# Kernel optimization log

Hardware: AMD Instinct MI355X
Metric: run time of the kernel (lower is better)

Reference implementation:

```python
import jax, jax.numpy as jnp
import numpy as np

B, L, H, NH = 2, 256, 512, 8
DH = H // NH
MAXLEN = 256           # module's max_seq_len; pe index offset
PE_ROWS = 2 * MAXLEN + 1


def _lin(x, W, b):
    # torch nn.Linear convention: y = x @ W.T + b
    return x @ W.T + b


def setup_inputs() -> dict:
    rng = jax.random.key(0)
    ks = jax.random.split(rng, 24)
    s = 0.02
    inp = {
        "key": jax.random.normal(ks[0], (B, L, H), jnp.float32),
        "query": jax.random.normal(ks[1], (B, L, H), jnp.float32),
        "value": jax.random.normal(ks[2], (B, L, H), jnp.float32),
        # learned params
        "pe": jax.random.normal(ks[3], (PE_ROWS, H), jnp.float32) * s,
        "Wf": jax.random.normal(ks[4], (H, 4 * H), jnp.float32) * s,
        "bf": jnp.zeros((H,), jnp.float32),
        "Wk": jax.random.normal(ks[5], (H, H), jnp.float32) * s,
        "bk": jnp.zeros((H,), jnp.float32),
        "Wq": jax.random.normal(ks[6], (H, H), jnp.float32) * s,
        "bq": jnp.zeros((H,), jnp.float32),
        "Wv": jax.random.normal(ks[7], (H, H), jnp.float32) * s,
        "bv": jnp.zeros((H,), jnp.float32),
        "Wr": jax.random.normal(ks[8], (H, H), jnp.float32) * s,
        "br": jnp.zeros((H,), jnp.float32),
        "Wo": jax.random.normal(ks[9], (H, H), jnp.float32) * s,  # ff_final
        "bo": jnp.zeros((H,), jnp.float32),
        "u": jax.random.normal(ks[10], (NH, DH), jnp.float32) * s,
        "v": jax.random.normal(ks[11], (NH, DH), jnp.float32) * s,
        # int inputs
        "seq_len": jax.random.randint(ks[12], (B,), 100, 200).astype(jnp.int64),
        "lex_num": jax.random.randint(ks[13], (B,), 0, 50).astype(jnp.int64),
    }
    pos_s = jax.random.randint(ks[14], (B, L), 0, 250)
    pos_e = pos_s + jax.random.randint(ks[15], (B, L), 0, 5)
    inp["pos_s"] = pos_s.astype(jnp.int64)
    inp["pos_e"] = pos_e.astype(jnp.int64)
    return inp


def reference(key, query, value, pe, Wf, bf, Wk, bk, Wq, bq, Wv, bv, Wr, br,
              Wo, bo, u, v, seq_len, lex_num, pos_s, pos_e):
    b, l, _ = key.shape
    # four relative position matrices [B, L, L]
    pos_ss = pos_s[:, :, None] - pos_s[:, None, :]
    pos_se = pos_s[:, :, None] - pos_e[:, None, :]
    pos_es = pos_e[:, :, None] - pos_s[:, None, :]
    pos_ee = pos_e[:, :, None] - pos_e[:, None, :]
    # gather pe embeddings, each [B, L, L, H]
    pe_ss = pe[pos_ss + MAXLEN]
    pe_se = pe[pos_se + MAXLEN]
    pe_es = pe[pos_es + MAXLEN]
    pe_ee = pe[pos_ee + MAXLEN]
    pe_4 = jnp.concatenate([pe_ss, pe_se, pe_es, pe_ee], axis=-1)  # [B,L,L,4H]
    rel = jax.nn.relu(_lin(pe_4, Wf, bf))                          # 'ff' fusion -> [B,L,L,H]

    q = _lin(query, Wq, bq).reshape(b, l, NH, DH).transpose(0, 2, 1, 3)  # [B,nh,L,dh]
    k = _lin(key, Wk, bk).reshape(b, l, NH, DH).transpose(0, 2, 1, 3)
    val = _lin(value, Wv, bv).reshape(b, l, NH, DH).transpose(0, 2, 1, 3)
    rel = _lin(rel, Wr, br).reshape(b, l, l, NH, DH)               # [B,L,L,nh,dh]

    A = jnp.einsum('bhid,bhjd->bhij', q, k)
    B_ = jnp.einsum('bhid,bijhd->bhij', q, rel)
    C = jnp.einsum('hd,bhjd->bhj', u, k)[:, :, None, :]
    D = jnp.einsum('hd,bijhd->bhij', v, rel)

    score = (A + B_ + C + D) / np.float32(np.sqrt(DH))
    total_len = seq_len + lex_num                                   # [B]
    mask = (jnp.arange(l)[None, :] < total_len[:, None])[:, None, None, :]
    score = jnp.where(mask, score, jnp.float32(-1e15))
    attn = jax.nn.softmax(score, axis=-1)
    out = jnp.einsum('bhij,bhjd->bhid', attn, val)                  # [B,nh,L,dh]
    out = out.transpose(0, 2, 1, 3).reshape(b, l, H)
    return _lin(out, Wo, bo)
```

## Files before the change

kernel.cpp:

```cpp
#include <hip/hip_runtime.h>
#include <hip/hip_bf16.h>

typedef unsigned short USHORT;
typedef long long LL;
typedef short s8v __attribute__((ext_vector_type(8)));
typedef float f32x4 __attribute__((ext_vector_type(4)));


__device__ __forceinline__ float bf2f(USHORT u) {
  union { unsigned int i; float f; } v; v.i = ((unsigned int)u) << 16; return v.f;
}
__device__ __forceinline__ USHORT f2bf(float f) {
  unsigned int x = __float_as_uint(f);
  return (USHORT)((x + 0x7fffu + ((x >> 16) & 1u)) >> 16);
}

struct PrepArgs {
  const void* fsrc[18]; USHORT* fdst[18]; int fn[18];
  const void* wr_src; USHORT* wrT;
  const void* isrc[4]; int* idst[4];
};

__global__ __launch_bounds__(256) void prep_k(PrepArgs a, const void* qraw, int* flags) {
  __shared__ int s_w;
  const int t = threadIdx.x;
  if (t == 0) s_w = 0;
  __syncthreads();
  const USHORT* qb = (const USHORT*)qraw;
  int wild = 0;
  for (int c = t; c < 512; c += 256) {
    float x = bf2f(qb[c]);
    if (!(fabsf(x) <= 1024.0f)) wild = 1;
  }
  if (wild) atomicAdd(&s_w, 1);
  __syncthreads();
  const int f = (s_w == 0) ? 1 : 0;

  const int y = blockIdx.y;
  if (y < 18) {
    const int n = a.fn[y];
    const USHORT* sb = (const USHORT*)a.fsrc[y];
    const float* sf = (const float*)a.fsrc[y];
    USHORT* d = a.fdst[y];
    for (int idx = blockIdx.x * 256 + t; idx < n; idx += gridDim.x * 256)
      d[idx] = f ? sb[idx] : f2bf(sf[idx]);
  } else if (y == 18) {
    const USHORT* sb = (const USHORT*)a.wr_src;
    const float* sf = (const float*)a.wr_src;
    for (int idx = blockIdx.x * 256 + t; idx < 262144; idx += gridDim.x * 256) {
      const int e = idx >> 9, dd = idx & 511;
      const int s = dd * 512 + e;
      a.wrT[idx] = f ? sb[s] : f2bf(sf[s]);
    }
  } else if (blockIdx.x == 0) {
    if (t == 0) flags[0] = f;
    const int fi = (((const int*)a.isrc[0])[1] == 0) ? 1 : 0;
    if (t < 2) {
      a.idst[0][t] = fi ? (int)((const LL*)a.isrc[0])[t] : ((const int*)a.isrc[0])[t];
      a.idst[1][t] = fi ? (int)((const LL*)a.isrc[1])[t] : ((const int*)a.isrc[1])[t];
    }
    for (int c = t; c < 512; c += 256) {
      a.idst[2][c] = fi ? (int)((const LL*)a.isrc[2])[c] : ((const int*)a.isrc[2])[c];
      a.idst[3][c] = fi ? (int)((const LL*)a.isrc[3])[c] : ((const int*)a.isrc[3])[c];
    }
  }
}

struct GDesc {
  const USHORT* A; const USHORT* W; const USHORT* bias;
  void* out;
  int M, N, K, lda, ldw, koff, ldo, mode, trans, pad;
};
struct GArgs { GDesc d[32]; };

__global__ __launch_bounds__(256) void gemm2_k(GArgs ga, const int* __restrict__ flags) {
  const GDesc de = ga.d[blockIdx.z];
  const int row0 = blockIdx.y * 64, col0 = blockIdx.x * 64;
  if (row0 >= de.M || col0 >= de.N) return;
  const int wave = threadIdx.x >> 6, lane = threadIdx.x & 63;
  const int mrow = row0 + wave * 16 + (lane & 15);
  const int kq = (lane >> 4) * 8;
  const bool mok = (mrow < de.M);
  const USHORT* ar = de.A + (long)(mok ? mrow : row0) * de.lda + kq;
  const int nc = col0 + (lane & 15);
  const USHORT* w0p = de.W + (long)(nc +  0) * de.ldw + de.koff + kq;
  const USHORT* w1p = de.W + (long)(nc + 16) * de.ldw + de.koff + kq;
  const USHORT* w2p = de.W + (long)(nc + 32) * de.ldw + de.koff + kq;
  const USHORT* w3p = de.W + (long)(nc + 48) * de.ldw + de.koff + kq;

  f32x4 acc[4] = {};
#pragma unroll 4
  for (int k0 = 0; k0 < de.K; k0 += 32) {
    s8v a = *(const s8v*)(ar + k0);
    s8v wv0 = *(const s8v*)(w0p + k0);
    s8v wv1 = *(const s8v*)(w1p + k0);
    s8v wv2 = *(const s8v*)(w2p + k0);
    s8v wv3 = *(const s8v*)(w3p + k0);
    acc[0] = __builtin_amdgcn_mfma_f32_16x16x32_bf16(a, wv0, acc[0], 0, 0, 0);
    acc[1] = __builtin_amdgcn_mfma_f32_16x16x32_bf16(a, wv1, acc[1], 0, 0, 0);
    acc[2] = __builtin_amdgcn_mfma_f32_16x16x32_bf16(a, wv2, acc[2], 0, 0, 0);
    acc[3] = __builtin_amdgcn_mfma_f32_16x16x32_bf16(a, wv3, acc[3], 0, 0, 0);
  }

  const int obf = (de.mode == 2) ? flags[0] : (de.mode == 1);
  const int mbase = row0 + wave * 16 + (lane >> 4) * 4;
#pragma unroll
  for (int nt = 0; nt < 4; nt++) {
    const int n = col0 + nt * 16 + (lane & 15);
    const float bias = de.bias ? bf2f(de.bias[n]) : 0.f;
#pragma unroll
    for (int r = 0; r < 4; r++) {
      const int m = mbase + r;
      if (m >= de.M) continue;
      const float vo = acc[nt][r] + bias;
      const long off = de.trans ? ((long)n * de.ldo + m) : ((long)m * de.ldo + n);
      if (obf) ((USHORT*)de.out)[off] = f2bf(vo);
      else     ((float*)de.out)[off] = vo;
    }
  }
}

__global__ __launch_bounds__(256) void mid_k(
    const USHORT* __restrict__ Ptab, const USHORT* __restrict__ q_n,
    const USHORT* __restrict__ k_n, const USHORT* __restrict__ WrT,
    const USHORT* __restrict__ u_bf, const USHORT* __restrict__ v_bf,
    const USHORT* __restrict__ br_bf,
    USHORT* __restrict__ T,
    float* __restrict__ cbv, float* __restrict__ uk, USHORT* __restrict__ vwr)
{
  const int bid = blockIdx.x, t = threadIdx.x, gsz = gridDim.x;
  const long TS = 513l * 512;
  for (int r = bid; r < 12825; r += gsz) {
    const int S0 = r / 25, rem = r % 25, di = rem / 5, dj = rem % 5;
    const USHORT* p1 = Ptab + (long)S0 * 512;
    const USHORT* p2 = Ptab + TS + (long)max(S0 - dj, 0) * 512;
    const USHORT* p3 = Ptab + 2 * TS + (long)min(S0 + di, 512) * 512;
    const USHORT* p4 = Ptab + 3 * TS + (long)min(max(S0 + di - dj, 0), 512) * 512;
    USHORT* to = T + (long)r * 512;
    const int e = t * 2;
    ushort2 x1 = *(const ushort2*)(p1 + e);
    ushort2 x2 = *(const ushort2*)(p2 + e);
    ushort2 x3 = *(const ushort2*)(p3 + e);
    ushort2 x4 = *(const ushort2*)(p4 + e);
    ushort2 o;
    o.x = f2bf(fmaxf(bf2f(x1.x) + bf2f(x2.x) + bf2f(x3.x) + bf2f(x4.x), 0.f));
    o.y = f2bf(fmaxf(bf2f(x1.y) + bf2f(x2.y) + bf2f(x3.y) + bf2f(x4.y), 0.f));
    *(ushort2*)(to + e) = o;
  }
  for (int idx = bid * 256 + t; idx < 262144; idx += gsz * 256) {
    const int hd = idx & 511;
    float s = (bf2f(q_n[idx]) + bf2f(v_bf[hd])) * bf2f(br_bf[hd]);
    float s2 = bf2f(k_n[idx]) * bf2f(u_bf[hd]);
#pragma unroll
    for (int off = 32; off > 0; off >>= 1) { s += __shfl_xor(s, off); s2 += __shfl_xor(s2, off); }
    if ((t & 63) == 0) { cbv[idx >> 6] = s; uk[idx >> 6] = s2; }
  }
  for (int o = bid * 256 + t; o < 4096; o += gsz * 256) {
    const int h = o >> 9, e = o & 511;
    float s = 0.f;
    const USHORT* wrow = WrT + (long)e * 512 + h * 64;
    const USHORT* vrow = v_bf + h * 64;
#pragma unroll
    for (int d = 0; d < 64; d += 4) {
      ushort4 wv = *(const ushort4*)(wrow + d);
      ushort4 vv = *(const ushort4*)(vrow + d);
      s += bf2f(vv.x) * bf2f(wv.x) + bf2f(vv.y) * bf2f(wv.y) +
           bf2f(vv.z) * bf2f(wv.z) + bf2f(vv.w) * bf2f(wv.w);
    }
    vwr[o] = f2bf(s);
  }
}

__global__ __launch_bounds__(256) void score5_k(
    const USHORT* __restrict__ T,
    const float* __restrict__ cbv, const float* __restrict__ uk,
    const USHORT* __restrict__ wbuf,
    const int* __restrict__ seq_len, const int* __restrict__ lex_num,
    const int* __restrict__ pos_s, const int* __restrict__ pos_e,
    float* __restrict__ S)
{
  const int i = blockIdx.x, b = blockIdx.y;
  const int wave = threadIdx.x >> 6, lane = threadIdx.x & 63;
  const int jt = blockIdx.z * 4 + wave;
  int tl = seq_len[b] + lex_num[b];
  tl = min(max(tl, 1), 256);
  const int j0 = jt * 16;
  if (j0 >= tl) return;
  const int n = lane & 15, q = lane >> 4;
  const int psi = pos_s[b * 256 + i], pei = pos_e[b * 256 + i];
  const int j = j0 + n;
  const int psj = pos_s[b * 256 + j], pej = pos_e[b * 256 + j];
  const int S0 = min(max(psi - psj + 256, 0), 512);
  const int di = min(max(pei - psi, 0), 4);
  const int dj = min(max(pej - psj, 0), 4);
  const USHORT* tp = T + ((long)(S0 * 25 + di * 5 + dj)) * 512 + q * 8;
  const USHORT* wr = wbuf + ((long)((b * 8 + (n & 7)) * 256 + i)) * 512 + q * 8;

  f32x4 acc = {0.f, 0.f, 0.f, 0.f};
#pragma unroll
  for (int kk = 0; kk < 16; kk++) {
    s8v av = *(const s8v*)(tp + kk * 32);
    s8v wv = *(const s8v*)(wr + kk * 32);
    acc = __builtin_amdgcn_mfma_f32_16x16x32_bf16(av, wv, acc, 0, 0, 0);
  }
  if (n < 8) {
    const long base = (long)(b * 8 + n) * 256 + i;
    const float cb = cbv[(long)(b * 256 + i) * 8 + n];
    float* dst = S + base * 256 + j0 + q * 4;
    const float4 sac = *(const float4*)dst;
    const float* sacp = (const float*)&sac;
#pragma unroll
    for (int r = 0; r < 4; r++) {
      const int jr = j0 + q * 4 + r;
      dst[r] = (acc[r] + sacp[r] + cb + uk[(long)(b * 256 + jr) * 8 + n]) * 0.125f;
    }
  }
}

__global__ __launch_bounds__(256) void softav_k(
    const float* __restrict__ S, const USHORT* __restrict__ v_t,
    const int* __restrict__ seq_len, const int* __restrict__ lex_num,
    USHORT* __restrict__ out_pre)
{
  __shared__ float att[8 * 256];
  __shared__ float red4[4];
  const int i = blockIdx.x, b = blockIdx.y, t = threadIdx.x;
  const int lane = t & 63, wave = t >> 6;
  int tl = seq_len[b] + lex_num[b];
  tl = min(max(tl, 1), 256);
  for (int h = 0; h < 8; h++) {
    const long base = ((long)(b * 8 + h) * 256 + i) * 256;
    const float val = (t < tl) ? S[base + t] : -3.0e38f;
    float m = val;
#pragma unroll
    for (int off = 32; off > 0; off >>= 1) m = fmaxf(m, __shfl_xor(m, off));
    if (lane == 0) red4[wave] = m;
    __syncthreads();
    m = fmaxf(fmaxf(red4[0], red4[1]), fmaxf(red4[2], red4[3]));
    const float pv = (t < tl) ? __expf(val - m) : 0.f;
    float s = pv;
#pragma unroll
    for (int off = 32; off > 0; off >>= 1) s += __shfl_xor(s, off);
    __syncthreads();
    if (lane == 0) red4[wave] = s;
    __syncthreads();
    s = red4[0] + red4[1] + red4[2] + red4[3];
    if (!(s > 1e-30f)) s = 1.f;
    att[h * 256 + t] = pv / s;
    __syncthreads();
  }
#pragma unroll
  for (int pass = 0; pass < 2; pass++) {
    const int h = (t >> 6) + 4 * pass;
    const int d = t & 63;
    const USHORT* vrow = v_t + (long)(h * 64 + d) * 512 + b * 256;
    const float* arow = &att[h * 256];
    float acc = 0.f;
    const int tl4 = (tl + 3) & ~3;
    for (int jj = 0; jj < tl4; jj += 4) {
      ushort4 vv = *(const ushort4*)(vrow + jj);
      acc += arow[jj + 0] * bf2f(vv.x) + arow[jj + 1] * bf2f(vv.y) +
             arow[jj + 2] * bf2f(vv.z) + arow[jj + 3] * bf2f(vv.w);
    }
    out_pre[(long)(b * 256 + i) * 512 + h * 64 + d] = f2bf(acc);
  }
}

extern "C" void kernel_launch(void* const* d_in, const int* in_sizes, int n_in,
                              void* d_out, int out_size, void* d_ws, size_t ws_size,
                              hipStream_t stream) {
  (void)in_sizes; (void)n_in; (void)out_size; (void)ws_size;

  char* w = (char*)d_ws;
  auto take = [&](size_t n) { char* r = w; w += (n + 255) & ~(size_t)255; return r; };

  int* flags   = (int*)take(16);
  int* c_seq   = (int*)take(16);
  int* c_lex   = (int*)take(16);
  int* c_pos_s = (int*)take(2048);
  int* c_pos_e = (int*)take(2048);
  const int ns[18] = {262144,262144,262144,262656,1048576,512,262144,512,262144,512,
                      262144,512,262144,512,262144,512,512,512};
  USHORT* canon[18];
  for (int i = 0; i < 18; i++) canon[i] = (USHORT*)take((size_t)ns[i] * 2);
  USHORT* WrT     = (USHORT*)take((size_t)262144 * 2);
  USHORT* q_n     = (USHORT*)take((size_t)262144 * 2);
  USHORT* k_n     = (USHORT*)take((size_t)262144 * 2);
  USHORT* v_t     = (USHORT*)take((size_t)262144 * 2);
  USHORT* wbuf    = (USHORT*)take((size_t)2097152 * 2);
  USHORT* Ptab    = (USHORT*)take((size_t)1050624 * 2);
  USHORT* T       = (USHORT*)take((size_t)12825 * 512 * 2);
  USHORT* vwr     = (USHORT*)take((size_t)4096 * 2);
  USHORT* out_pre = (USHORT*)take((size_t)262144 * 2);
  float* S   = (float*)take((size_t)1048576 * 4);
  float* cbv = (float*)take((size_t)4096 * 4);
  float* uk  = (float*)take((size_t)4096 * 4);

  PrepArgs pa;
  for (int i = 0; i < 18; i++) { pa.fsrc[i] = d_in[i]; pa.fdst[i] = canon[i]; pa.fn[i] = ns[i]; }
  pa.wr_src = d_in[12]; pa.wrT = WrT;
  for (int i = 0; i < 4; i++) pa.isrc[i] = d_in[18 + i];
  pa.idst[0] = c_seq; pa.idst[1] = c_lex; pa.idst[2] = c_pos_s; pa.idst[3] = c_pos_e;
  prep_k<<<dim3(64, 20), 256, 0, stream>>>(pa, d_in[1], flags);

  GArgs gA = {};
  for (int z = 0; z < 4; z++)
    gA.d[z] = {canon[3], canon[4], (z == 0) ? canon[5] : nullptr, Ptab + (long)z * 513 * 512,
               513, 512, 512, 512, 2048, z * 512, 512, 1, 0, 0};
  gA.d[4] = {canon[1], canon[8],  canon[9],  q_n, 512, 512, 512, 512, 512, 0, 512, 1, 0, 0};
  gA.d[5] = {canon[0], canon[6],  canon[7],  k_n, 512, 512, 512, 512, 512, 0, 512, 1, 0, 0};
  gA.d[6] = {canon[2], canon[10], canon[11], v_t, 512, 512, 512, 512, 512, 0, 512, 1, 1, 0};
  gemm2_k<<<dim3(8, 9, 7), 256, 0, stream>>>(gA, flags);

  mid_k<<<512, 256, 0, stream>>>(Ptab, q_n, k_n, WrT, canon[16], canon[17], canon[13],
                                 T, cbv, uk, vwr);

  GArgs gB = {};
  for (int z = 0; z < 16; z++) {
    const int b = z >> 3, h = z & 7;
    gB.d[z] = {q_n + b * 131072 + h * 64, WrT, vwr + h * 512, wbuf + (long)z * 131072,
               256, 512, 64, 512, 512, h * 64, 512, 1, 0, 0};
  }
  for (int z = 0; z < 16; z++) {
    const int b = z >> 3, h = z & 7;
    gB.d[16 + z] = {q_n + b * 131072 + h * 64, k_n + b * 131072 + h * 64, nullptr,
                    S + (long)z * 65536, 256, 256, 64, 512, 512, 0, 256, 0, 0, 0};
  }
  gemm2_k<<<dim3(8, 4, 32), 256, 0, stream>>>(gB, flags);

  score5_k<<<dim3(256, 2, 4), 256, 0, stream>>>(
      T, cbv, uk, wbuf, c_seq, c_lex, c_pos_s, c_pos_e, S);

  softav_k<<<dim3(256, 2), 256, 0, stream>>>(S, v_t, c_seq, c_lex, out_pre);

  GArgs gC = {};
  gC.d[0] = {out_pre, canon[14], canon[15], d_out, 512, 512, 512, 512, 512, 0, 512, 2, 0, 0};
  gemm2_k<<<dim3(8, 8, 1), 256, 0, stream>>>(gC, flags);
}
```

Before: 223.2 us.

## Fuse relative-position score MFMA with softmax and attention-value product in one kernel

Merges the score kernel and the softmax/AV kernel into a single 1024-thread block per (query row, batch). The 16 waves compute all 256 key columns of the B+D term with MFMA, add the A+C partials and write scaled scores straight into shared memory. Softmax and the value product then run from LDS, so the full score matrix is never written back and reread from global memory, and one launch is removed. The cost is a larger block with more barriers and fewer blocks (512) to spread across the GPU.

```diff
diff --git a/kernel.cpp b/kernel.cpp
--- a/kernel.cpp
+++ b/kernel.cpp
@@ -171,88 +171,80 @@
   }
 }
 
-__global__ __launch_bounds__(256) void score5_k(
+__global__ __launch_bounds__(1024) void score6_k(
     const USHORT* __restrict__ T,
     const float* __restrict__ cbv, const float* __restrict__ uk,
-    const USHORT* __restrict__ wbuf,
+    const USHORT* __restrict__ wbuf, const float* __restrict__ S_AC,
+    const USHORT* __restrict__ v_t,
     const int* __restrict__ seq_len, const int* __restrict__ lex_num,
     const int* __restrict__ pos_s, const int* __restrict__ pos_e,
-    float* __restrict__ S)
-{
-  const int i = blockIdx.x, b = blockIdx.y;
-  const int wave = threadIdx.x >> 6, lane = threadIdx.x & 63;
-  const int jt = blockIdx.z * 4 + wave;
-  int tl = seq_len[b] + lex_num[b];
-  tl = min(max(tl, 1), 256);
-  const int j0 = jt * 16;
-  if (j0 >= tl) return;
-  const int n = lane & 15, q = lane >> 4;
-  const int psi = pos_s[b * 256 + i], pei = pos_e[b * 256 + i];
-  const int j = j0 + n;
-  const int psj = pos_s[b * 256 + j], pej = pos_e[b * 256 + j];
-  const int S0 = min(max(psi - psj + 256, 0), 512);
-  const int di = min(max(pei - psi, 0), 4);
-  const int dj = min(max(pej - psj, 0), 4);
-  const USHORT* tp = T + ((long)(S0 * 25 + di * 5 + dj)) * 512 + q * 8;
-  const USHORT* wr = wbuf + ((long)((b * 8 + (n & 7)) * 256 + i)) * 512 + q * 8;
-
-  f32x4 acc = {0.f, 0.f, 0.f, 0.f};
-#pragma unroll
-  for (int kk = 0; kk < 16; kk++) {
-    s8v av = *(const s8v*)(tp + kk * 32);
-    s8v wv = *(const s8v*)(wr + kk * 32);
-    acc = __builtin_amdgcn_mfma_f32_16x16x32_bf16(av, wv, acc, 0, 0, 0);
-  }
-  if (n < 8) {
-    const long base = (long)(b * 8 + n) * 256 + i;
-    const float cb = cbv[(long)(b * 256 + i) * 8 + n];
-    float* dst = S + base * 256 + j0 + q * 4;
-    const float4 sac = *(const float4*)dst;
-    const float* sacp = (const float*)&sac;
-#pragma unroll
-    for (int r = 0; r < 4; r++) {
-      const int jr = j0 + q * 4 + r;
-      dst[r] = (acc[r] + sacp[r] + cb + uk[(long)(b * 256 + jr) * 8 + n]) * 0.125f;
-    }
-  }
-}
-
-__global__ __launch_bounds__(256) void softav_k(
-    const float* __restrict__ S, const USHORT* __restrict__ v_t,
-    const int* __restrict__ seq_len, const int* __restrict__ lex_num,
     USHORT* __restrict__ out_pre)
 {
   __shared__ float att[8 * 256];
-  __shared__ float red4[4];
+  __shared__ float red[4][4];
   const int i = blockIdx.x, b = blockIdx.y, t = threadIdx.x;
-  const int lane = t & 63, wave = t >> 6;
+  const int wave = t >> 6, lane = t & 63;
   int tl = seq_len[b] + lex_num[b];
   tl = min(max(tl, 1), 256);
-  for (int h = 0; h < 8; h++) {
-    const long base = ((long)(b * 8 + h) * 256 + i) * 256;
-    const float val = (t < tl) ? S[base + t] : -3.0e38f;
+
+  const int j0 = wave * 16;
+  if (j0 < tl) {
+    const int n = lane & 15, q = lane >> 4;
+    const int psi = pos_s[b * 256 + i], pei = pos_e[b * 256 + i];
+    const int j = j0 + n;
+    const int psj = pos_s[b * 256 + j], pej = pos_e[b * 256 + j];
+    const int S0 = min(max(psi - psj + 256, 0), 512);
+    const int di = min(max(pei - psi, 0), 4);
+    const int dj = min(max(pej - psj, 0), 4);
+    const USHORT* tp = T + ((long)(S0 * 25 + di * 5 + dj)) * 512 + q * 8;
+    const USHORT* wr = wbuf + ((long)((b * 8 + (n & 7)) * 256 + i)) * 512 + q * 8;
+    f32x4 acc = {0.f, 0.f, 0.f, 0.f};
+#pragma unroll
+    for (int kk = 0; kk < 16; kk++) {
+      s8v av = *(const s8v*)(tp + kk * 32);
+      s8v wv = *(const s8v*)(wr + kk * 32);
+      acc = __builtin_amdgcn_mfma_f32_16x16x32_bf16(av, wv, acc, 0, 0, 0);
+    }
+    if (n < 8) {
+      const long base = (long)(b * 8 + n) * 256 + i;
+      const float cb = cbv[(long)(b * 256 + i) * 8 + n];
+      const float4 sac = *(const float4*)(S_AC + base * 256 + j0 + q * 4);
+      const float* sacp = (const float*)&sac;
+#pragma unroll
+      for (int r = 0; r < 4; r++) {
+        const int jr = j0 + q * 4 + r;
+        att[n * 256 + jr] = (acc[r] + sacp[r] + cb + uk[(long)(b * 256 + jr) * 8 + n]) * 0.125f;
+      }
+    }
+  }
+  __syncthreads();
+
+  const int hg = t >> 8, tj = t & 255, wig = wave & 3;
+#pragma unroll
+  for (int hh = 0; hh < 2; hh++) {
+    const int h = hg + 4 * hh;
+    const float val = (tj < tl) ? att[h * 256 + tj] : -3.0e38f;
     float m = val;
 #pragma unroll
     for (int off = 32; off > 0; off >>= 1) m = fmaxf(m, __shfl_xor(m, off));
-    if (lane == 0) red4[wave] = m;
+    if (lane == 0) red[hg][wig] = m;
     __syncthreads();
-    m = fmaxf(fmaxf(red4[0], red4[1]), fmaxf(red4[2], red4[3]));
-    const float pv = (t < tl) ? __expf(val - m) : 0.f;
+    m = fmaxf(fmaxf(red[hg][0], red[hg][1]), fmaxf(red[hg][2], red[hg][3]));
+    const float pv = (tj < tl) ? __expf(val - m) : 0.f;
     float s = pv;
 #pragma unroll
     for (int off = 32; off > 0; off >>= 1) s += __shfl_xor(s, off);
     __syncthreads();
-    if (lane == 0) red4[wave] = s;
+    if (lane == 0) red[hg][wig] = s;
     __syncthreads();
-    s = red4[0] + red4[1] + red4[2] + red4[3];
+    s = red[hg][0] + red[hg][1] + red[hg][2] + red[hg][3];
     if (!(s > 1e-30f)) s = 1.f;
-    att[h * 256 + t] = pv / s;
+    att[h * 256 + tj] = pv / s;
     __syncthreads();
   }
-#pragma unroll
-  for (int pass = 0; pass < 2; pass++) {
-    const int h = (t >> 6) + 4 * pass;
-    const int d = t & 63;
+
+  if (t < 512) {
+    const int h = t >> 6, d = t & 63;
     const USHORT* vrow = v_t + (long)(h * 64 + d) * 512 + b * 256;
     const float* arow = &att[h * 256];
     float acc = 0.f;
@@ -328,10 +320,8 @@
   }
   gemm2_k<<<dim3(8, 4, 32), 256, 0, stream>>>(gB, flags);
 
-  score5_k<<<dim3(256, 2, 4), 256, 0, stream>>>(
-      T, cbv, uk, wbuf, c_seq, c_lex, c_pos_s, c_pos_e, S);
-
-  softav_k<<<dim3(256, 2), 256, 0, stream>>>(S, v_t, c_seq, c_lex, out_pre);
+  score6_k<<<dim3(256, 2), 1024, 0, stream>>>(
+      T, cbv, uk, wbuf, S, v_t, c_seq, c_lex, c_pos_s, c_pos_e, out_pre);
 
   GArgs gC = {};
   gC.d[0] = {out_pre, canon[14], canon[15], d_out, 512, 512, 512, 512, 512, 0, 512, 2, 0, 0};
```

Measured after the change: 216.8 us, median of 2. 2.9% less time.
